# Optimization experiments

Hardware: AMD Instinct MI355X
Metric: run time of the kernel (lower is better)

The kernel has to match this reference:

```python
import jax, jax.numpy as jnp
import numpy as np

N = 100000   # nodes (in_ch)
D = 128      # emb_ch
E = 1600000  # nonzeros in A_hat
RATE = 0.1   # dropout rate


def setup_inputs() -> dict:
    key = jax.random.key(0)
    k1, k2, k3, k4, k5, k6 = jax.random.split(key, 6)
    x = jnp.arange(N, dtype=jnp.int64) if jax.config.jax_enable_x64 else jnp.arange(N, dtype=jnp.int32)
    rows = jax.random.randint(k1, (E,), 0, N)
    cols = jax.random.randint(k2, (E,), 0, N)
    A_vals = jax.random.uniform(k3, (E,), dtype=jnp.float32)
    # xavier_uniform for [N, D]: bound = sqrt(6/(N+D))
    bound = float(np.sqrt(6.0 / (N + D)))
    emb_weight = jax.random.uniform(k4, (N, D), jnp.float32, -bound, bound)
    u1 = jax.random.uniform(k5, (N, D), dtype=jnp.float32)
    u2 = jax.random.uniform(k6, (N, D), dtype=jnp.float32)
    return {"x": x, "rows": rows, "cols": cols, "A_vals": A_vals,
            "emb_weight": emb_weight, "u1": u1, "u2": u2}


def _dropout(h, u):
    keep = (u >= RATE).astype(h.dtype)
    return h * keep / (1.0 - RATE)


def _spmm(rows, cols, vals, h):
    # out[i] = sum_{e: rows[e]==i} vals[e] * h[cols[e]]  -- COO SpMM
    msgs = vals[:, None] * h[cols]  # [E, D]
    return jax.ops.segment_sum(msgs, rows, num_segments=N)


def reference(x, rows, cols, A_vals, emb_weight, u1, u2):
    h0 = emb_weight[x]                       # embedding lookup [N, D]
    h1 = _spmm(rows, cols, A_vals, _dropout(h0, u1))
    h2 = _spmm(rows, cols, A_vals, _dropout(h1, u2))
    return (h0 + h1 + h2) / 3.0
```

## Files before the change

kernel.cpp:

```cpp
#include <hip/hip_runtime.h>
#include <hip/hip_fp16.h>

#define DD 128
#define SCAN_CHUNK 1024
#define G_ROWS 32
#define G_STAGE 1024
#define NCOPY 8

typedef float          f32x4 __attribute__((ext_vector_type(4)));
typedef unsigned int   u32x4 __attribute__((ext_vector_type(4)));
typedef unsigned int   u32x2 __attribute__((ext_vector_type(2)));
typedef unsigned short u16x8 __attribute__((ext_vector_type(8)));

struct __align__(8) Edge { int c; float v; };

__device__ __forceinline__ unsigned short f2h(float f) {
    return __half_as_ushort(__float2half(f));
}
__device__ __forceinline__ float2 up2(unsigned int u) {
    __half2 h = *reinterpret_cast<const __half2*>(&u);
    return __half22float2(h);
}

template <typename T>
__device__ __forceinline__ T ldnt(const T* p) { return __builtin_nontemporal_load(p); }
template <typename T>
__device__ __forceinline__ void stnt(T* p, T v) { __builtin_nontemporal_store(v, p); }

__global__ __launch_bounds__(256) void k_g1hist(const float* __restrict__ emb,
                                                const float* __restrict__ u1,
                                                ushort* __restrict__ g1,
                                                const int* __restrict__ rows,
                                                int* __restrict__ cnt8,
                                                ushort* __restrict__ rank,
                                                int total8, int E, int N) {
    int i = blockIdx.x * 256 + threadIdx.x;
    int k = blockIdx.x & (NCOPY - 1);
    bool doE = i < E;
    bool doS = i < total8;
    int r = 0;
    if (doE) r = ldnt(rows + i);
    f32x4 hA, hB, uA, uB;
    if (doS) {
        const f32x4* e4 = (const f32x4*)emb;
        const f32x4* a4 = (const f32x4*)u1;
        hA = ldnt(e4 + 2 * (size_t)i);
        hB = ldnt(e4 + 2 * (size_t)i + 1);
        uA = ldnt(a4 + 2 * (size_t)i);
        uB = ldnt(a4 + 2 * (size_t)i + 1);
    }
    if (doE) {
        int old = atomicAdd(&cnt8[(size_t)k * N + r], 1);
        stnt(rank + i, (ushort)((k << 13) | old));
    }
    if (doS) {
        const float s = 1.0f / 0.9f;
        u16x8 g;
        g[0] = f2h((uA.x >= 0.1f) ? hA.x * s : 0.0f);
        g[1] = f2h((uA.y >= 0.1f) ? hA.y * s : 0.0f);
        g[2] = f2h((uA.z >= 0.1f) ? hA.z * s : 0.0f);
        g[3] = f2h((uA.w >= 0.1f) ? hA.w * s : 0.0f);
        g[4] = f2h((uB.x >= 0.1f) ? hB.x * s : 0.0f);
        g[5] = f2h((uB.y >= 0.1f) ? hB.y * s : 0.0f);
        g[6] = f2h((uB.z >= 0.1f) ? hB.z * s : 0.0f);
        g[7] = f2h((uB.w >= 0.1f) ? hB.w * s : 0.0f);
        ((u16x8*)g1)[i] = g;
    }
}

__global__ __launch_bounds__(256) void k_scan1(int* __restrict__ cnt8,
                                               int* __restrict__ rs,
                                               int* __restrict__ bsum, int n) {
    __shared__ int s[256];
    int tid = threadIdx.x;
    int base = blockIdx.x * SCAN_CHUNK + tid * 4;
    int c[4][NCOPY];
    int tot[4];
#pragma unroll
    for (int j = 0; j < 4; ++j) {
        int row = base + j;
        int t = 0;
        if (row < n) {
#pragma unroll
            for (int k = 0; k < NCOPY; ++k) {
                c[j][k] = cnt8[(size_t)k * n + row];
                t += c[j][k];
            }
        }
        tot[j] = t;
    }
    int tsum = tot[0] + tot[1] + tot[2] + tot[3];
    s[tid] = tsum;
    __syncthreads();
    for (int off = 1; off < 256; off <<= 1) {
        int t = (tid >= off) ? s[tid - off] : 0;
        __syncthreads();
        s[tid] += t;
        __syncthreads();
    }
    int excl = s[tid] - tsum;
    if (tid == 255) bsum[blockIdx.x] = s[255];
    int run = excl;
#pragma unroll
    for (int j = 0; j < 4; ++j) {
        int row = base + j;
        if (row < n) {
            rs[row] = run;
            int p = run;
#pragma unroll
            for (int k = 0; k < NCOPY; ++k) {
                cnt8[(size_t)k * n + row] = p;
                p += c[j][k];
            }
        }
        run += tot[j];
    }
}

__global__ __launch_bounds__(256) void k_scan23(int* __restrict__ rs,
                                                int* __restrict__ cnt8,
                                                const int* __restrict__ bsum,
                                                int nb, int n) {
    __shared__ int s[1024];
    int tid = threadIdx.x;
    for (int i = tid; i < nb; i += 256) s[i] = bsum[i];
    __syncthreads();
    if (tid == 0) {
        int run = 0;
        for (int i = 0; i < nb; ++i) { int t = s[i]; s[i] = run; run += t; }
    }
    __syncthreads();
    int i = blockIdx.x * 256 + tid;
    if (i < n) {
        int off = s[i >> 10];
        rs[i] += off;
#pragma unroll
        for (int k = 0; k < NCOPY; ++k) cnt8[(size_t)k * n + i] += off;
    }
}

__global__ __launch_bounds__(256) void k_scatter_prep(const int* __restrict__ rows,
                                                      const int* __restrict__ cols,
                                                      const float* __restrict__ vals,
                                                      const int* __restrict__ cnt8,
                                                      const ushort* __restrict__ rank,
                                                      Edge* __restrict__ ev,
                                                      const float* __restrict__ emb,
                                                      const float* __restrict__ u2,
                                                      ushort* __restrict__ emb16,
                                                      unsigned char* __restrict__ mask2,
                                                      int E, int total8, int N) {
    int i = blockIdx.x * 256 + threadIdx.x;
    bool doE = i < E;
    bool doS = i < total8;
    int r = 0, c = 0; float vv = 0.f; unsigned int rk = 0;
    if (doE) {
        r = ldnt(rows + i);
        c = ldnt(cols + i);
        vv = ldnt(vals + i);
        rk = ldnt(rank + i);
    }
    f32x4 hA, hB, vA, vB;
    if (doS) {
        const f32x4* e4 = (const f32x4*)emb;
        const f32x4* b4 = (const f32x4*)u2;
        hA = ldnt(e4 + 2 * (size_t)i);
        hB = ldnt(e4 + 2 * (size_t)i + 1);
        vA = ldnt(b4 + 2 * (size_t)i);
        vB = ldnt(b4 + 2 * (size_t)i + 1);
    }
    if (doE) {
        int kk = rk >> 13;
        int rin = rk & 0x1FFF;
        int pos = cnt8[(size_t)kk * N + r] + rin;
        u32x2 q;
        q.x = (unsigned int)c;
        q.y = __float_as_uint(vv);
        ((u32x2*)ev)[pos] = q;
    }
    if (doS) {
        u16x8 e16;
        e16[0] = f2h(hA.x); e16[1] = f2h(hA.y); e16[2] = f2h(hA.z); e16[3] = f2h(hA.w);
        e16[4] = f2h(hB.x); e16[5] = f2h(hB.y); e16[6] = f2h(hB.z); e16[7] = f2h(hB.w);
        stnt((u16x8*)emb16 + i, e16);
        unsigned char m =
            (unsigned char)((vA.x >= 0.1f ? 1u : 0u)  | (vA.y >= 0.1f ? 2u : 0u)  |
                            (vA.z >= 0.1f ? 4u : 0u)  | (vA.w >= 0.1f ? 8u : 0u)  |
                            (vB.x >= 0.1f ? 16u : 0u) | (vB.y >= 0.1f ? 32u : 0u) |
                            (vB.z >= 0.1f ? 64u : 0u) | (vB.w >= 0.1f ? 128u : 0u));
        stnt(mask2 + i, m);
    }
}

template <int MODE>
__global__ __launch_bounds__(256) void k_gather(const int* __restrict__ rowstart,
                                                const Edge* __restrict__ ev,
                                                const ushort* __restrict__ srch,
                                                const unsigned char* __restrict__ mask2,
                                                const ushort* __restrict__ emb16,
                                                const ushort* __restrict__ p16in,
                                                ushort* __restrict__ p16out,
                                                ushort* __restrict__ g2,
                                                float* __restrict__ out,
                                                int N, int E) {
    __shared__ int s_rs[G_ROWS + 1];
    __shared__ Edge s_ev[G_STAGE];

    int tid = threadIdx.x;
    int r0 = blockIdx.x * G_ROWS;
    int h = blockIdx.y;
    if (tid <= G_ROWS) {
        int r = r0 + tid;
        s_rs[tid] = (r < N) ? rowstart[r] : E;
    }
    __syncthreads();
    int base = s_rs[0];
    int nblk = s_rs[G_ROWS] - base;
    int nstage = nblk < G_STAGE ? nblk : G_STAGE;
    for (int i = tid; i < nstage; i += 256) {
        u32x2 q = ldnt((const u32x2*)(ev + base + i));
        Edge ed; ed.c = (int)q.x; ed.v = __uint_as_float(q.y);
        s_ev[i] = ed;
    }
    __syncthreads();

    int grp = tid >> 3;
    int lane = tid & 7;
    int row = r0 + grp;
    if (row >= N) return;
    int start = s_rs[grp] - base;
    int end = s_rs[grp + 1] - base;
    int eL = end < nstage ? end : nstage;

    const u32x4* __restrict__ s4 = (const u32x4*)srch;
    const Edge* __restrict__ evg = ev + base;
    int hoff = (h << 3) + lane;
    float a0 = 0.f, a1 = 0.f, a2 = 0.f, a3 = 0.f;
    float a4 = 0.f, a5 = 0.f, a6 = 0.f, a7 = 0.f;

#define LDE(i) Edge E##i = s_ev[e + i]; float fv##i = E##i.v;
#define LDP(i) int ix##i = e + i; bool ok##i = ix##i < eL; \
               Edge E##i = s_ev[ok##i ? ix##i : last]; \
               float fv##i = ok##i ? E##i.v : 0.0f;
#define GQ(i)  u32x4 q##i = s4[((size_t)E##i.c << 4) + hoff];
#define ACC(i) { float vv = fv##i; \
        float2 w0 = up2(q##i.x), w1 = up2(q##i.y), w2 = up2(q##i.z), w3 = up2(q##i.w); \
        a0 = fmaf(vv, w0.x, a0); a1 = fmaf(vv, w0.y, a1); \
        a2 = fmaf(vv, w1.x, a2); a3 = fmaf(vv, w1.y, a3); \
        a4 = fmaf(vv, w2.x, a4); a5 = fmaf(vv, w2.y, a5); \
        a6 = fmaf(vv, w3.x, a6); a7 = fmaf(vv, w3.y, a7); }

    int e = start;
    for (; e + 8 <= eL; e += 8) {
        LDE(0) LDE(1) LDE(2) LDE(3) LDE(4) LDE(5) LDE(6) LDE(7)
        GQ(0) GQ(1) GQ(2) GQ(3) GQ(4) GQ(5) GQ(6) GQ(7)
        ACC(0) ACC(1) ACC(2) ACC(3) ACC(4) ACC(5) ACC(6) ACC(7)
    }
    if (e < eL) {
        int last = eL - 1;
        LDP(0) LDP(1) LDP(2) LDP(3) LDP(4) LDP(5) LDP(6) LDP(7)
        GQ(0) GQ(1) GQ(2) GQ(3) GQ(4) GQ(5) GQ(6) GQ(7)
        ACC(0) ACC(1) ACC(2) ACC(3) ACC(4) ACC(5) ACC(6) ACC(7)
        e = eL;
    }
    for (; e < end; ++e) {
        Edge E0; { u32x2 q_ = ldnt((const u32x2*)(evg + e));
                   E0.c = (int)q_.x; E0.v = __uint_as_float(q_.y); }
        float fv0 = E0.v;
        GQ(0) ACC(0)
    }
#undef LDE
#undef LDP
#undef GQ
#undef ACC

    size_t o = ((size_t)row << 7) + ((size_t)h << 6) + (size_t)lane * 8;
    if (MODE == 1) {
        unsigned int m = mask2[(size_t)row * 16 + (h << 3) + lane];
        const float s = 1.0f / 0.9f;
        u16x8 gg;
        gg[0] = (m & 1u)   ? f2h(a0 * s) : (ushort)0;
        gg[1] = (m & 2u)   ? f2h(a1 * s) : (ushort)0;
        gg[2] = (m & 4u)   ? f2h(a2 * s) : (ushort)0;
        gg[3] = (m & 8u)   ? f2h(a3 * s) : (ushort)0;
        gg[4] = (m & 16u)  ? f2h(a4 * s) : (ushort)0;
        gg[5] = (m & 32u)  ? f2h(a5 * s) : (ushort)0;
        gg[6] = (m & 64u)  ? f2h(a6 * s) : (ushort)0;
        gg[7] = (m & 128u) ? f2h(a7 * s) : (ushort)0;
        stnt((u16x8*)(g2 + o), gg);
        u16x8 pp;
        pp[0] = f2h(a0); pp[1] = f2h(a1); pp[2] = f2h(a2); pp[3] = f2h(a3);
        pp[4] = f2h(a4); pp[5] = f2h(a5); pp[6] = f2h(a6); pp[7] = f2h(a7);
        stnt((u16x8*)(p16out + o), pp);
    } else {
        u32x4 eq = ldnt((const u32x4*)(emb16 + o));
        u32x4 pq = ldnt((const u32x4*)(p16in + o));
        float2 e0 = up2(eq.x), e1 = up2(eq.y), e2 = up2(eq.z), e3 = up2(eq.w);
        float2 p0 = up2(pq.x), p1 = up2(pq.y), p2 = up2(pq.z), p3 = up2(pq.w);
        const float t3 = 1.0f / 3.0f;
        f32x4 rA, rB;
        rA.x = (e0.x + p0.x + a0) * t3;
        rA.y = (e0.y + p0.y + a1) * t3;
        rA.z = (e1.x + p1.x + a2) * t3;
        rA.w = (e1.y + p1.y + a3) * t3;
        rB.x = (e2.x + p2.x + a4) * t3;
        rB.y = (e2.y + p2.y + a5) * t3;
        rB.z = (e3.x + p3.x + a6) * t3;
        rB.w = (e3.y + p3.y + a7) * t3;
        stnt((f32x4*)(out + o), rA);
        stnt((f32x4*)(out + o) + 1, rB);
    }
}


extern "C" void kernel_launch(void* const* d_in, const int* in_sizes, int n_in,
                              void* d_out, int out_size, void* d_ws, size_t ws_size,
                              hipStream_t stream) {
    const int* rows = (const int*)d_in[1];
    const int* cols = (const int*)d_in[2];
    const float* vals = (const float*)d_in[3];
    const float* emb = (const float*)d_in[4];
    const float* u1 = (const float*)d_in[5];
    const float* u2 = (const float*)d_in[6];
    float* out = (float*)d_out;

    const int N = in_sizes[0];
    const int E = in_sizes[1];
    const size_t ND = (size_t)N * DD;

    char* ws = (char*)d_ws;
    Edge* ev     = (Edge*)ws;   ws += (size_t)E * sizeof(Edge);
    ushort* g1   = (ushort*)ws; ws += ND * sizeof(ushort);
    ushort* g2   = (ushort*)ws; ws += ND * sizeof(ushort);
    ushort* p16  = (ushort*)ws; ws += ND * sizeof(ushort);
    ushort* emb16= (ushort*)ws; ws += ND * sizeof(ushort);
    int* cnt8    = (int*)ws;    ws += (size_t)NCOPY * N * sizeof(int);
    int* rs      = (int*)ws;    ws += (size_t)N * sizeof(int);
    ushort* rank = (ushort*)ws; ws += (size_t)E * sizeof(ushort);
    int* bsum    = (int*)ws;    ws += 4096;
    unsigned char* mask2 = (unsigned char*)ws;

    const int total8 = (int)(ND / 8);
    const int prepBlocks = (total8 + 255) / 256;
    const int gridE = (E + 255) / 256;
    const int gridFuse = prepBlocks > gridE ? prepBlocks : gridE;
    const int nScanBlocks = (N + SCAN_CHUNK - 1) / SCAN_CHUNK;
    const int gridRowX = (N + G_ROWS - 1) / G_ROWS;
    dim3 gridRow(gridRowX, 2, 1);

    hipMemsetAsync(cnt8, 0, (size_t)NCOPY * N * sizeof(int), stream);
    k_g1hist<<<gridFuse, 256, 0, stream>>>(emb, u1, g1, rows, cnt8, rank,
                                           total8, E, N);
    k_scan1<<<nScanBlocks, 256, 0, stream>>>(cnt8, rs, bsum, N);
    k_scan23<<<(N + 255) / 256, 256, 0, stream>>>(rs, cnt8, bsum, nScanBlocks, N);
    k_scatter_prep<<<gridFuse, 256, 0, stream>>>(rows, cols, vals, cnt8, rank,
                                                 ev, emb, u2, emb16, mask2,
                                                 E, total8, N);
    k_gather<1><<<gridRow, 256, 0, stream>>>(rs, ev, g1, mask2, nullptr, nullptr,
                                             p16, g2, nullptr, N, E);
    k_gather<2><<<gridRow, 256, 0, stream>>>(rs, ev, g2, nullptr, emb16, p16,
                                             nullptr, nullptr, out, N, E);
}
```

Before: 403.7 us.

## Replace 8-copy histogram with packed 16-bit per-row counters

Replaces the 8 replicated int counter arrays, which spread atomic contention across copies, with a single array of packed 16-bit counters, two rows per 32-bit word. The scan kernels no longer read and write the eight copies, and the scatter computes each edge position directly from the row start plus its rank. This cuts the memset, scan traffic and counter footprint, at the cost of more atomic contention per word because there are no copies and adjacent rows share a word. It also assumes no row's degree exceeds 65535.

```diff
diff --git a/kernel.cpp b/kernel.cpp
--- a/kernel.cpp
+++ b/kernel.cpp
@@ -5,7 +5,6 @@
 #define SCAN_CHUNK 1024
 #define G_ROWS 32
 #define G_STAGE 1024
-#define NCOPY 8
 
 typedef float          f32x4 __attribute__((ext_vector_type(4)));
 typedef unsigned int   u32x4 __attribute__((ext_vector_type(4)));
@@ -31,11 +30,10 @@
                                                 const float* __restrict__ u1,
                                                 ushort* __restrict__ g1,
                                                 const int* __restrict__ rows,
-                                                int* __restrict__ cnt8,
+                                                unsigned int* __restrict__ cnt16,
                                                 ushort* __restrict__ rank,
-                                                int total8, int E, int N) {
+                                                int total8, int E) {
     int i = blockIdx.x * 256 + threadIdx.x;
-    int k = blockIdx.x & (NCOPY - 1);
     bool doE = i < E;
     bool doS = i < total8;
     int r = 0;
@@ -50,8 +48,9 @@
         uB = ldnt(a4 + 2 * (size_t)i + 1);
     }
     if (doE) {
-        int old = atomicAdd(&cnt8[(size_t)k * N + r], 1);
-        stnt(rank + i, (ushort)((k << 13) | old));
+        int sh = (r & 1) << 4;
+        unsigned int old = atomicAdd(&cnt16[r >> 1], 1u << sh);
+        stnt(rank + i, (ushort)((old >> sh) & 0xFFFFu));
     }
     if (doS) {
         const float s = 1.0f / 0.9f;
@@ -68,28 +67,24 @@
     }
 }
 
-__global__ __launch_bounds__(256) void k_scan1(int* __restrict__ cnt8,
+__global__ __launch_bounds__(256) void k_scan1(const unsigned int* __restrict__ cnt16,
                                                int* __restrict__ rs,
                                                int* __restrict__ bsum, int n) {
     __shared__ int s[256];
     int tid = threadIdx.x;
     int base = blockIdx.x * SCAN_CHUNK + tid * 4;
-    int c[4][NCOPY];
-    int tot[4];
-#pragma unroll
-    for (int j = 0; j < 4; ++j) {
-        int row = base + j;
-        int t = 0;
-        if (row < n) {
-#pragma unroll
-            for (int k = 0; k < NCOPY; ++k) {
-                c[j][k] = cnt8[(size_t)k * n + row];
-                t += c[j][k];
-            }
-        }
-        tot[j] = t;
-    }
-    int tsum = tot[0] + tot[1] + tot[2] + tot[3];
+    int c0 = 0, c1 = 0, c2 = 0, c3 = 0;
+    if (base < n) {
+        unsigned int w0 = cnt16[base >> 1];
+        c0 = (int)(w0 & 0xFFFFu);
+        c1 = (int)(w0 >> 16);
+    }
+    if (base + 2 < n) {
+        unsigned int w1 = cnt16[(base >> 1) + 1];
+        c2 = (int)(w1 & 0xFFFFu);
+        c3 = (int)(w1 >> 16);
+    }
+    int tsum = c0 + c1 + c2 + c3;
     s[tid] = tsum;
     __syncthreads();
     for (int off = 1; off < 256; off <<= 1) {
@@ -100,25 +95,13 @@
     }
     int excl = s[tid] - tsum;
     if (tid == 255) bsum[blockIdx.x] = s[255];
-    int run = excl;
-#pragma unroll
-    for (int j = 0; j < 4; ++j) {
-        int row = base + j;
-        if (row < n) {
-            rs[row] = run;
-            int p = run;
-#pragma unroll
-            for (int k = 0; k < NCOPY; ++k) {
-                cnt8[(size_t)k * n + row] = p;
-                p += c[j][k];
-            }
-        }
-        run += tot[j];
-    }
+    if (base < n)     rs[base]     = excl;
+    if (base + 1 < n) rs[base + 1] = excl + c0;
+    if (base + 2 < n) rs[base + 2] = excl + c0 + c1;
+    if (base + 3 < n) rs[base + 3] = excl + c0 + c1 + c2;
 }
 
 __global__ __launch_bounds__(256) void k_scan23(int* __restrict__ rs,
-                                                int* __restrict__ cnt8,
                                                 const int* __restrict__ bsum,
                                                 int nb, int n) {
     __shared__ int s[1024];
@@ -131,25 +114,20 @@
     }
     __syncthreads();
     int i = blockIdx.x * 256 + tid;
-    if (i < n) {
-        int off = s[i >> 10];
-        rs[i] += off;
-#pragma unroll
-        for (int k = 0; k < NCOPY; ++k) cnt8[(size_t)k * n + i] += off;
-    }
+    if (i < n) rs[i] += s[i >> 10];
 }
 
 __global__ __launch_bounds__(256) void k_scatter_prep(const int* __restrict__ rows,
                                                       const int* __restrict__ cols,
                                                       const float* __restrict__ vals,
-                                                      const int* __restrict__ cnt8,
+                                                      const int* __restrict__ rs,
                                                       const ushort* __restrict__ rank,
                                                       Edge* __restrict__ ev,
                                                       const float* __restrict__ emb,
                                                       const float* __restrict__ u2,
                                                       ushort* __restrict__ emb16,
                                                       unsigned char* __restrict__ mask2,
-                                                      int E, int total8, int N) {
+                                                      int E, int total8) {
     int i = blockIdx.x * 256 + threadIdx.x;
     bool doE = i < E;
     bool doS = i < total8;
@@ -170,9 +148,7 @@
         vB = ldnt(b4 + 2 * (size_t)i + 1);
     }
     if (doE) {
-        int kk = rk >> 13;
-        int rin = rk & 0x1FFF;
-        int pos = cnt8[(size_t)kk * N + r] + rin;
+        int pos = rs[r] + (int)rk;
         u32x2 q;
         q.x = (unsigned int)c;
         q.y = __float_as_uint(vv);
@@ -327,6 +303,7 @@
     const int N = in_sizes[0];
     const int E = in_sizes[1];
     const size_t ND = (size_t)N * DD;
+    const int NW = (N + 1) / 2;
 
     char* ws = (char*)d_ws;
     Edge* ev     = (Edge*)ws;   ws += (size_t)E * sizeof(Edge);
@@ -334,7 +311,7 @@
     ushort* g2   = (ushort*)ws; ws += ND * sizeof(ushort);
     ushort* p16  = (ushort*)ws; ws += ND * sizeof(ushort);
     ushort* emb16= (ushort*)ws; ws += ND * sizeof(ushort);
-    int* cnt8    = (int*)ws;    ws += (size_t)NCOPY * N * sizeof(int);
+    unsigned int* cnt16 = (unsigned int*)ws; ws += (size_t)NW * 4;
     int* rs      = (int*)ws;    ws += (size_t)N * sizeof(int);
     ushort* rank = (ushort*)ws; ws += (size_t)E * sizeof(ushort);
     int* bsum    = (int*)ws;    ws += 4096;
@@ -348,14 +325,14 @@
     const int gridRowX = (N + G_ROWS - 1) / G_ROWS;
     dim3 gridRow(gridRowX, 2, 1);
 
-    hipMemsetAsync(cnt8, 0, (size_t)NCOPY * N * sizeof(int), stream);
-    k_g1hist<<<gridFuse, 256, 0, stream>>>(emb, u1, g1, rows, cnt8, rank,
-                                           total8, E, N);
-    k_scan1<<<nScanBlocks, 256, 0, stream>>>(cnt8, rs, bsum, N);
-    k_scan23<<<(N + 255) / 256, 256, 0, stream>>>(rs, cnt8, bsum, nScanBlocks, N);
-    k_scatter_prep<<<gridFuse, 256, 0, stream>>>(rows, cols, vals, cnt8, rank,
+    hipMemsetAsync(cnt16, 0, (size_t)NW * 4, stream);
+    k_g1hist<<<gridFuse, 256, 0, stream>>>(emb, u1, g1, rows, cnt16, rank,
+                                           total8, E);
+    k_scan1<<<nScanBlocks, 256, 0, stream>>>(cnt16, rs, bsum, N);
+    k_scan23<<<(N + 255) / 256, 256, 0, stream>>>(rs, bsum, nScanBlocks, N);
+    k_scatter_prep<<<gridFuse, 256, 0, stream>>>(rows, cols, vals, rs, rank,
                                                  ev, emb, u2, emb16, mask2,
-                                                 E, total8, N);
+                                                 E, total8);
     k_gather<1><<<gridRow, 256, 0, stream>>>(rs, ev, g1, mask2, nullptr, nullptr,
                                              p16, g2, nullptr, N, E);
     k_gather<2><<<gridRow, 256, 0, stream>>>(rs, ev, g2, nullptr, emb16, p16,
```

New measurement: 404.2 us (median of 2 runs). About the same (+0.1%).
